# Kernel tuning notes

Measured on AMD Instinct MI355X. Metric: run time of the kernel, lower is better.

Reference implementation:

```python
import math
import jax, jax.numpy as jnp
import numpy as np

B, L, HID, NHEADS, HEAD_DIM = 4, 2048, 1024, 16, 64


def setup_inputs() -> dict:
    key = jax.random.key(0)
    ks = jax.random.split(key, 11)
    s = 1.0 / math.sqrt(HID)
    f32 = jnp.float32
    inp = {
        "query": jax.random.normal(ks[0], (B, L, HID), dtype=f32),
        "key": jax.random.normal(ks[1], (B, L, HID), dtype=f32),
        "val": jax.random.normal(ks[2], (B, L, HID), dtype=f32),
        # causal multiplicative 0/1 mask; module adds attn_mask.log()
        "attn_mask": jnp.tril(jnp.ones((1, L, L), dtype=f32)),
        "Wq": jax.random.normal(ks[3], (HID, HID), dtype=f32) * s,
        "bq": jnp.zeros((HID,), dtype=f32),
        "Wk": jax.random.normal(ks[4], (HID, HID), dtype=f32) * s,
        "bk": jnp.zeros((HID,), dtype=f32),
        "Wv": jax.random.normal(ks[5], (HID, HID), dtype=f32) * s,
        "bv": jnp.zeros((HID,), dtype=f32),
        "Wo": jax.random.normal(ks[6], (HID, HID), dtype=f32) * s,
        "bo": jnp.zeros((HID,), dtype=f32),
    }
    return inp


def _mha(query, key, val, attn_mask, Wq, bq, Wk, bk, Wv, bv, Wo, bo):
    # projections (torch Linear: x @ W.T + b), then split heads
    q = (query @ Wq.T + bq).reshape(B, L, NHEADS, HEAD_DIM)
    k = (key @ Wk.T + bk).reshape(B, L, NHEADS, HEAD_DIM)
    v = (val @ Wv.T + bv).reshape(B, L, NHEADS, HEAD_DIM)
    # scores: [B, H, Lq, Lk]
    logits = jnp.einsum("blhd,bmhd->bhlm", q, k)
    # faithful order: add log(mask) BEFORE scaling by 1/sqrt(head_dim)
    logits = logits + jnp.log(attn_mask)[:, None, :, :]
    logits = logits / math.sqrt(HEAD_DIM)
    attn = jax.nn.softmax(logits, axis=-1)  # -inf rows handled by softmax
    out = jnp.einsum("bhlm,bmhd->blhd", attn, v).reshape(B, L, HID)
    return out @ Wo.T + bo


def reference(query, key, val, attn_mask, Wq, bq, Wk, bk, Wv, bv, Wo, bo):
    return _mha(query, key, val, attn_mask, Wq, bq, Wk, bk, Wv, bv, Wo, bo)
```

## Files before the change

kernel.cpp:

```cpp
#include <hip/hip_runtime.h>
#include <hip/hip_bf16.h>
#include <stdint.h>

#define L_SEQ 2048
#define HID   1024
#define NH    16
#define HD    64
#define MTOT  8192

typedef __bf16 bf16;
typedef bf16  bf16x8 __attribute__((ext_vector_type(8)));
typedef float f32x4  __attribute__((ext_vector_type(4)));
typedef uint32_t u32x4 __attribute__((ext_vector_type(4)));

#define NEG_BIG (-1e30f)
#define F32_PROBE 0x3F800000u

__device__ __forceinline__ uint32_t pack_bf16(float x, float y) {
    unsigned short a = __builtin_bit_cast(unsigned short, (bf16)x);
    unsigned short b = __builtin_bit_cast(unsigned short, (bf16)y);
    return (uint32_t)a | ((uint32_t)b << 16);
}

__device__ __forceinline__ bf16x8 cvt8(float4 a, float4 b) {
    bf16x8 r;
    r[0] = (bf16)a.x; r[1] = (bf16)a.y; r[2] = (bf16)a.z; r[3] = (bf16)a.w;
    r[4] = (bf16)b.x; r[5] = (bf16)b.y; r[6] = (bf16)b.z; r[7] = (bf16)b.w;
    return r;
}

__device__ __forceinline__ bf16x8 load8(const void* p, size_t off, bool is_f32) {
    if (is_f32) {
        const float4* f = (const float4*)((const float*)p + off);
        return cvt8(f[0], f[1]);
    }
    return *(const bf16x8*)((const bf16*)p + off);
}

__device__ __forceinline__ void load_lds16(const bf16* g, bf16* l) {
    __builtin_amdgcn_global_load_lds(
        (const __attribute__((address_space(1))) unsigned int*)g,
        (__attribute__((address_space(3))) unsigned int*)l,
        16, 0, 0);
}

__global__ __launch_bounds__(256)
void cvt_to_bf16(const void* __restrict__ src, bf16* __restrict__ dst,
                 const uint32_t* __restrict__ probe)
{
    const bool f = (probe[0] == F32_PROBE);
    const size_t i = ((size_t)blockIdx.x * 256 + threadIdx.x) * 8;
    *(bf16x8*)(dst + i) = load8(src, i, f);
}

__global__ __launch_bounds__(256)
void cvt_w4(const void* __restrict__ w0, const void* __restrict__ w1,
            const void* __restrict__ w2, const void* __restrict__ w3,
            bf16* __restrict__ dst, const uint32_t* __restrict__ probe)
{
    const bool f = (probe[0] == F32_PROBE);
    const int t = blockIdx.x >> 9;
    const void* src = (t == 0) ? w0 : (t == 1) ? w1 : (t == 2) ? w2 : w3;
    const size_t i = ((size_t)(blockIdx.x & 511) * 256 + threadIdx.x) * 8;
    *(bf16x8*)(dst + (size_t)t * HID * HID + i) = load8(src, i, f);
}

__global__ __launch_bounds__(256)
void gemm_bt(const bf16* __restrict__ A, const bf16* __restrict__ W,
             const void* __restrict__ bias, void* __restrict__ C,
             const uint32_t* __restrict__ probe, int mode)
{
    const bool in_f32 = (probe[0] == F32_PROBE);
    const int K = 1024;
    __shared__ bf16 sA[128 * 32];
    __shared__ bf16 sB[128 * 32];
    const int tid  = threadIdx.x;
    const int lane = tid & 63;
    const int wid  = tid >> 6;
    const int m0 = blockIdx.y * 128;
    const int n0 = blockIdx.x * 128;
    const int wm = (wid & 1) * 64;
    const int wn = (wid >> 1) * 64;
    const int lrow = lane & 15;
    const int quad = lane >> 4;

    const int srow = tid >> 2;
    const int sseg = (tid & 3) * 8;
    const bf16* gA0 = A + (size_t)(m0 + srow) * K + sseg;
    const bf16* gA1 = gA0 + (size_t)64 * K;
    const bf16* gW0 = W + (size_t)(n0 + srow) * K + sseg;
    const bf16* gW1 = gW0 + (size_t)64 * K;
    bf16* lA0 = &sA[tid * 8];
    bf16* lA1 = lA0 + 64 * 32;
    bf16* lB0 = &sB[tid * 8];
    bf16* lB1 = lB0 + 64 * 32;

    f32x4 acc[4][4];
#pragma unroll
    for (int i = 0; i < 4; i++)
#pragma unroll
        for (int j = 0; j < 4; j++) acc[i][j] = (f32x4)0.0f;

    for (int kt = 0; kt < K; kt += 32) {
        load_lds16(gA0 + kt, lA0);
        load_lds16(gA1 + kt, lA1);
        load_lds16(gW0 + kt, lB0);
        load_lds16(gW1 + kt, lB1);
        __syncthreads();
        bf16x8 af[4], bw[4];
#pragma unroll
        for (int mt = 0; mt < 4; mt++)
            af[mt] = *(const bf16x8*)&sA[(wm + mt * 16 + lrow) * 32 + quad * 8];
#pragma unroll
        for (int nt = 0; nt < 4; nt++)
            bw[nt] = *(const bf16x8*)&sB[(wn + nt * 16 + lrow) * 32 + quad * 8];
#pragma unroll
        for (int mt = 0; mt < 4; mt++)
#pragma unroll
            for (int nt = 0; nt < 4; nt++)
                acc[mt][nt] = __builtin_amdgcn_mfma_f32_16x16x32_bf16(
                    af[mt], bw[nt], acc[mt][nt], 0, 0, 0);
        __syncthreads();
    }

#pragma unroll
    for (int nt = 0; nt < 4; nt++) {
        const int n = n0 + wn + nt * 16 + lrow;
        const float bv = in_f32 ? ((const float*)bias)[n]
                                : (float)((const bf16*)bias)[n];
#pragma unroll
        for (int mt = 0; mt < 4; mt++) {
#pragma unroll
            for (int i = 0; i < 4; i++) {
                const int m = m0 + wm + mt * 16 + quad * 4 + i;
                const float v = acc[mt][nt][i] + bv;
                if (mode == 0) {
                    ((float*)C)[(size_t)m * HID + n] = v;
                } else {
                    const int b = m >> 11, l = m & 2047;
                    const int h = n >> 6,  d = n & 63;
                    ((bf16*)C)[((size_t)(b * NH + h) * L_SEQ + l) * HD + d] = (bf16)v;
                }
            }
        }
    }
}

__global__ __launch_bounds__(256, 2)
void attn_fused(const bf16* __restrict__ Qw, const bf16* __restrict__ Kw,
                const bf16* __restrict__ Vw, bf16* __restrict__ ATT)
{
    const int tid  = threadIdx.x;
    const int lane = tid & 63;
    const int wid  = tid >> 6;
    const int idx  = blockIdx.x * 4 + wid;
    const int bh   = idx & 63;
    const int p    = idx >> 6;
    const int g    = (p & 1) ? (31 - (p >> 1)) : (p >> 1);
    const int q0   = g * 64;
    const int lrow = lane & 15;
    const int quad = lane >> 4;

    const bf16* Qb = Qw + (size_t)bh * (L_SEQ * HD);
    const bf16* Kb = Kw + (size_t)bh * (L_SEQ * HD);
    const bf16* Vb = Vw + (size_t)bh * (L_SEQ * HD);

    bf16x8 qf[4][2];
#pragma unroll
    for (int s = 0; s < 4; s++) {
        const bf16* qp = &Qb[(size_t)(q0 + 16 * s + lrow) * HD + quad * 8];
        qf[s][0] = *(const bf16x8*)(qp);
        qf[s][1] = *(const bf16x8*)(qp + 32);
    }

    f32x4 oacc[4][4];
#pragma unroll
    for (int s = 0; s < 4; s++)
#pragma unroll
        for (int dt = 0; dt < 4; dt++) oacc[s][dt] = (f32x4)0.0f;
    float l_lane[4] = {0.0f, 0.0f, 0.0f, 0.0f};
    const float cs = 0.18033688011112042f;
    const float msub = 8.0f;

    const int ntiles = 2 * g + 2;

    const bf16* kp0 = &Kb[(size_t)lrow * HD + quad * 8];
    bf16x8 ka0 = *(const bf16x8*)(kp0);
    bf16x8 ka1 = *(const bf16x8*)(kp0 + 32);
    bf16x8 kc0 = *(const bf16x8*)(kp0 + 16 * HD);
    bf16x8 kc1 = *(const bf16x8*)(kp0 + 16 * HD + 32);

    for (int t = 0; t < ntiles; t++) {
        const int kb = t * 32;

        bf16x8 vf0, vf1, vf2, vf3;
#pragma unroll
        for (int j = 0; j < 8; j++) {
            const bf16* vp = Vb + (size_t)(kb + quad * 8 + j) * HD + lrow;
            vf0[j] = vp[0];
            vf1[j] = vp[16];
            vf2[j] = vp[32];
            vf3[j] = vp[48];
        }
        const int kbn = (t + 1 < ntiles) ? kb + 32 : kb;
        const bf16* kpn = &Kb[(size_t)(kbn + lrow) * HD + quad * 8];
        const bf16x8 nk0 = *(const bf16x8*)(kpn);
        const bf16x8 nk1 = *(const bf16x8*)(kpn + 32);
        const bf16x8 nk2 = *(const bf16x8*)(kpn + 16 * HD);
        const bf16x8 nk3 = *(const bf16x8*)(kpn + 16 * HD + 32);

        const bool diag = (t >= 2 * g);
#pragma unroll
        for (int s = 0; s < 4; s++) {
            f32x4 sa = (f32x4)0.0f, sb = (f32x4)0.0f;
            sa = __builtin_amdgcn_mfma_f32_16x16x32_bf16(ka0, qf[s][0], sa, 0, 0, 0);
            sa = __builtin_amdgcn_mfma_f32_16x16x32_bf16(ka1, qf[s][1], sa, 0, 0, 0);
            sb = __builtin_amdgcn_mfma_f32_16x16x32_bf16(kc0, qf[s][0], sb, 0, 0, 0);
            sb = __builtin_amdgcn_mfma_f32_16x16x32_bf16(kc1, qf[s][1], sb, 0, 0, 0);

            float pa[4], pb[4];
            if (diag) {
                const int qr = q0 + 16 * s + lrow;
#pragma unroll
                for (int i = 0; i < 4; i++) {
                    const float taa = (kb + quad * 4 + i > qr)      ? NEG_BIG
                                      : __builtin_fmaf(sa[i], cs, -msub);
                    const float tbb = (kb + 16 + quad * 4 + i > qr) ? NEG_BIG
                                      : __builtin_fmaf(sb[i], cs, -msub);
                    pa[i] = exp2f(taa);
                    pb[i] = exp2f(tbb);
                }
            } else {
#pragma unroll
                for (int i = 0; i < 4; i++) {
                    pa[i] = exp2f(__builtin_fmaf(sa[i], cs, -msub));
                    pb[i] = exp2f(__builtin_fmaf(sb[i], cs, -msub));
                }
            }
#pragma unroll
            for (int i = 0; i < 4; i++) l_lane[s] += pa[i] + pb[i];

            const uint32_t ua0 = pack_bf16(pa[0], pa[1]);
            const uint32_t ua1 = pack_bf16(pa[2], pa[3]);
            const uint32_t ub0 = pack_bf16(pb[0], pb[1]);
            const uint32_t ub1 = pack_bf16(pb[2], pb[3]);
            const int srcA = lrow + (((quad * 2) & 3) << 4);
            const int srcB = lrow + (((quad * 2 + 1) & 3) << 4);
            const uint32_t va0 = (uint32_t)__shfl((int)ua0, srcA);
            const uint32_t va1 = (uint32_t)__shfl((int)ua1, srcA);
            const uint32_t wa0 = (uint32_t)__shfl((int)ua0, srcB);
            const uint32_t wa1 = (uint32_t)__shfl((int)ua1, srcB);
            const uint32_t vc0 = (uint32_t)__shfl((int)ub0, srcA);
            const uint32_t vc1 = (uint32_t)__shfl((int)ub1, srcA);
            const uint32_t wc0 = (uint32_t)__shfl((int)ub0, srcB);
            const uint32_t wc1 = (uint32_t)__shfl((int)ub1, srcB);
            const bool lo = quad < 2;
            u32x4 pw;
            pw.x = lo ? va0 : vc0;
            pw.y = lo ? va1 : vc1;
            pw.z = lo ? wa0 : wc0;
            pw.w = lo ? wa1 : wc1;
            const bf16x8 pfrag = __builtin_bit_cast(bf16x8, pw);

            oacc[s][0] = __builtin_amdgcn_mfma_f32_16x16x32_bf16(pfrag, vf0, oacc[s][0], 0, 0, 0);
            oacc[s][1] = __builtin_amdgcn_mfma_f32_16x16x32_bf16(pfrag, vf1, oacc[s][1], 0, 0, 0);
            oacc[s][2] = __builtin_amdgcn_mfma_f32_16x16x32_bf16(pfrag, vf2, oacc[s][2], 0, 0, 0);
            oacc[s][3] = __builtin_amdgcn_mfma_f32_16x16x32_bf16(pfrag, vf3, oacc[s][3], 0, 0, 0);
        }

        ka0 = nk0; ka1 = nk1; kc0 = nk2; kc1 = nk3;
    }

    const int b = bh >> 4, h = bh & 15;
#pragma unroll
    for (int s = 0; s < 4; s++) {
        float lr = l_lane[s];
        lr += __shfl_xor(lr, 16);
        lr += __shfl_xor(lr, 32);
        float li[4];
#pragma unroll
        for (int i = 0; i < 4; i++) li[i] = __shfl(lr, quad * 4 + i);
#pragma unroll
        for (int dt = 0; dt < 4; dt++) {
#pragma unroll
            for (int i = 0; i < 4; i++) {
                const int qrow = q0 + 16 * s + quad * 4 + i;
                const int d = dt * 16 + lrow;
                ATT[((size_t)(b * L_SEQ + qrow)) * HID + h * HD + d] =
                    (bf16)(oacc[s][dt][i] / li[i]);
            }
        }
    }
}

extern "C" void kernel_launch(void* const* d_in, const int* in_sizes, int n_in,
                              void* d_out, int out_size, void* d_ws, size_t ws_size,
                              hipStream_t stream) {
    (void)in_sizes; (void)n_in; (void)out_size; (void)ws_size;
    const void* query = d_in[0];
    const void* key   = d_in[1];
    const void* val   = d_in[2];
    const uint32_t* probe = (const uint32_t*)d_in[3];
    const void* Wq = d_in[4];
    const void* bq = d_in[5];
    const void* Wk = d_in[6];
    const void* bk = d_in[7];
    const void* Wv = d_in[8];
    const void* bv = d_in[9];
    const void* Wo = d_in[10];
    const void* bo = d_in[11];

    bf16* X0 = (bf16*)d_ws;
    bf16* Wb = X0 + (size_t)MTOT * HID;
    bf16* Kw = Wb + (size_t)4 * HID * HID;
    bf16* Vw = Kw + (size_t)MTOT * HID;
    bf16* Qw = (bf16*)d_out;
    const size_t WSTRIDE = (size_t)HID * HID;

    dim3 g(HID / 128, MTOT / 128);
    cvt_w4<<<2048, 256, 0, stream>>>(Wq, Wk, Wv, Wo, Wb, probe);
    cvt_to_bf16<<<MTOT * HID / 8 / 256, 256, 0, stream>>>(query, X0, probe);
    gemm_bt<<<g, 256, 0, stream>>>(X0, Wb + 0 * WSTRIDE, bq, Qw, probe, 1);
    cvt_to_bf16<<<MTOT * HID / 8 / 256, 256, 0, stream>>>(key, X0, probe);
    gemm_bt<<<g, 256, 0, stream>>>(X0, Wb + 1 * WSTRIDE, bk, Kw, probe, 1);
    cvt_to_bf16<<<MTOT * HID / 8 / 256, 256, 0, stream>>>(val, X0, probe);
    gemm_bt<<<g, 256, 0, stream>>>(X0, Wb + 2 * WSTRIDE, bv, Vw, probe, 1);
    attn_fused<<<512, 256, 0, stream>>>(Qw, Kw, Vw, X0);
    gemm_bt<<<g, 256, 0, stream>>>(X0, Wb + 3 * WSTRIDE, bo, d_out, probe, 0);
}
```

Baseline: 412.4 us.

## Use wave-private double-buffered LDS tiles in projection GEMM, drop block barriers

Each of the four waves now loads its own 64-row A and W slices into a private LDS region. The region is double-buffered so the next K-step's global-to-LDS loads are issued before the current step's MFMAs, and both __syncthreads barriers are replaced by a per-wave waitcnt. The aim is to hide load latency and remove block-wide synchronisation. In exchange, tiles that waves used to share are now fetched redundantly, roughly doubling global/L2 traffic per block. LDS per block also grows to 64KB, which can limit how many blocks fit on a CU.

```diff
diff --git a/kernel.cpp b/kernel.cpp
--- a/kernel.cpp
+++ b/kernel.cpp
@@ -72,8 +72,7 @@
 {
     const bool in_f32 = (probe[0] == F32_PROBE);
     const int K = 1024;
-    __shared__ bf16 sA[128 * 32];
-    __shared__ bf16 sB[128 * 32];
+    __shared__ bf16 smem[32768];
     const int tid  = threadIdx.x;
     const int lane = tid & 63;
     const int wid  = tid >> 6;
@@ -84,16 +83,12 @@
     const int lrow = lane & 15;
     const int quad = lane >> 4;
 
-    const int srow = tid >> 2;
-    const int sseg = (tid & 3) * 8;
-    const bf16* gA0 = A + (size_t)(m0 + srow) * K + sseg;
-    const bf16* gA1 = gA0 + (size_t)64 * K;
-    const bf16* gW0 = W + (size_t)(n0 + srow) * K + sseg;
-    const bf16* gW1 = gW0 + (size_t)64 * K;
-    bf16* lA0 = &sA[tid * 8];
-    bf16* lA1 = lA0 + 64 * 32;
-    bf16* lB0 = &sB[tid * 8];
-    bf16* lB1 = lB0 + 64 * 32;
+    const int srow = lane >> 2;
+    const int sseg = (lane & 3) * 8;
+    const bf16* gA = A + (size_t)(m0 + wm + srow) * K + sseg;
+    const bf16* gW = W + (size_t)(n0 + wn + srow) * K + sseg;
+    bf16* wbase = smem + wid * 8192;
+    bf16* ldst  = wbase + lane * 8;
 
     f32x4 acc[4][4];
 #pragma unroll
@@ -101,26 +96,39 @@
 #pragma unroll
         for (int j = 0; j < 4; j++) acc[i][j] = (f32x4)0.0f;
 
+#pragma unroll
+    for (int c = 0; c < 4; c++) {
+        load_lds16(gA + (size_t)(c * 16) * K, ldst + c * 512);
+        load_lds16(gW + (size_t)(c * 16) * K, ldst + 2048 + c * 512);
+    }
+
     for (int kt = 0; kt < K; kt += 32) {
-        load_lds16(gA0 + kt, lA0);
-        load_lds16(gA1 + kt, lA1);
-        load_lds16(gW0 + kt, lB0);
-        load_lds16(gW1 + kt, lB1);
-        __syncthreads();
+        const int buf = (kt >> 5) & 1;
+        bf16* cur = wbase + buf * 4096;
+        __builtin_amdgcn_s_waitcnt(0);
+        if (kt + 32 < K) {
+            bf16* nd = ldst + (buf ^ 1) * 4096;
+            const bf16* nA = gA + kt + 32;
+            const bf16* nW = gW + kt + 32;
+#pragma unroll
+            for (int c = 0; c < 4; c++) {
+                load_lds16(nA + (size_t)(c * 16) * K, nd + c * 512);
+                load_lds16(nW + (size_t)(c * 16) * K, nd + 2048 + c * 512);
+            }
+        }
         bf16x8 af[4], bw[4];
 #pragma unroll
         for (int mt = 0; mt < 4; mt++)
-            af[mt] = *(const bf16x8*)&sA[(wm + mt * 16 + lrow) * 32 + quad * 8];
+            af[mt] = *(const bf16x8*)&cur[(mt * 16 + lrow) * 32 + quad * 8];
 #pragma unroll
         for (int nt = 0; nt < 4; nt++)
-            bw[nt] = *(const bf16x8*)&sB[(wn + nt * 16 + lrow) * 32 + quad * 8];
+            bw[nt] = *(const bf16x8*)&cur[2048 + (nt * 16 + lrow) * 32 + quad * 8];
 #pragma unroll
         for (int mt = 0; mt < 4; mt++)
 #pragma unroll
             for (int nt = 0; nt < 4; nt++)
                 acc[mt][nt] = __builtin_amdgcn_mfma_f32_16x16x32_bf16(
                     af[mt], bw[nt], acc[mt][nt], 0, 0, 0);
-        __syncthreads();
     }
 
 #pragma unroll
```

Result: slower. 440.0 us (+6.7%).
